# Kernel tuning notes

Measured on AMD Instinct MI355X. Metric: run time of the kernel, lower is better.

The kernel has to match this reference:

```python
import jax, jax.numpy as jnp
import numpy as np

N_ORDERS = 2
CHUNK = 64            # real tokens per chunk
LINEAR_ACTIVATION = False
STAB = 10000.0


def _ensure_stability(x):
    x = jnp.clip(x, -STAB, STAB)
    return jnp.nan_to_num(x, nan=0.0, posinf=STAB, neginf=-STAB)


def setup_inputs() -> dict:
    key = jax.random.key(0)
    k1, k2, k3, k4 = jax.random.split(key, 4)
    B, H, NC, D = 2, 16, 32, 128
    CT = CHUNK * N_ORDERS  # 128 virtual tokens per chunk
    s = 1.0 / np.sqrt(D)
    q_chunks = jax.random.normal(k1, (B, H, NC, CT, D), jnp.float32) * s
    W = jax.random.normal(k2, (B, H, NC, CT, D), jnp.float32) * s
    U = jax.random.normal(k3, (B, H, NC, CT, D), jnp.float32) * s
    h0 = jax.random.normal(k4, (B, H, D, D), jnp.float32) * s
    return {"q_chunks": q_chunks, "W": W, "U": U, "h0": h0}


def _gelu_norm(h):
    # h_norm/2 * gelu(2*h/h_norm, tanh) applied to chunk-boundary state
    n = jnp.linalg.norm(h, axis=-1, keepdims=True) + 1e-6
    return n / 2.0 * jax.nn.gelu(2.0 * h / n, approximate=True)


def _delta_product_scan(q_chunks, W, U, h0):
    B, H, NC, CT, D = q_chunks.shape
    C = CT // N_ORDERS

    def body(h, chunk):
        q_c, w_c, u_c = chunk  # each [B,H,CT,D]
        # virtual-token layout: token c, step s lives at index c*n_orders+s
        qs = q_c.reshape(B, H, C, N_ORDERS, D)
        ws = w_c.reshape(B, H, C, N_ORDERS, D)
        us = u_c.reshape(B, H, C, N_ORDERS, D)
        state = jnp.broadcast_to(h[:, :, None], (B, H, C, D, D))  # per-token state
        outs = []
        for step in range(N_ORDERS):
            q_s = qs[:, :, :, step]
            w_s = ws[:, :, :, step]
            u_s = us[:, :, :, step]
            k_trans_h = jnp.einsum('bhcd,bhcde->bhce', w_s, state)
            u_val = u_s - k_trans_h
            o_inter = jnp.einsum('bhcd,bhcde->bhce', q_s, state)
            o_intra = q_s * u_val  # elementwise, as in source
            outs.append(o_intra + o_inter)
            state = _ensure_stability(state + w_s[..., :, None] * u_val[..., None, :])
        out = jnp.stack(outs, axis=3).reshape(B, H, CT, D)
        h_new = state[:, :, -1]
        if not LINEAR_ACTIVATION:
            h_new = _gelu_norm(h_new)
        return h_new, out

    chunks = (jnp.moveaxis(q_chunks, 2, 0), jnp.moveaxis(W, 2, 0), jnp.moveaxis(U, 2, 0))
    h_final, ys = jax.lax.scan(body, h0, chunks)
    return jnp.moveaxis(ys, 0, 2), h_final  # [B,H,NC,CT,D], [B,H,D,D]


def reference(q_chunks, W, U, h0):
    return _delta_product_scan(q_chunks, W, U, h0)
```

## Files before the change

kernel.cpp:

```cpp
#include <hip/hip_runtime.h>


#define Dd 128
#define NCH 32
#define YS 16777216

typedef __attribute__((ext_vector_type(4))) float floatx4;
typedef __attribute__((ext_vector_type(8))) short short8;

__device__ __forceinline__ unsigned cvtpk(float lo, float hi) {
  unsigned r;
  asm("v_cvt_pk_bf16_f32 %0, %1, %2" : "=v"(r) : "v"(lo), "v"(hi));
  return r;
}

__global__ __launch_bounds__(512) void p1_scan(const float* __restrict__ W,
    const float* __restrict__ U, const float* __restrict__ h0,
    unsigned short* __restrict__ hws, float* __restrict__ out) {
  __shared__ float wpre[NCH * 320];
  __shared__ float upre[NCH * 2 * Dd];
  __shared__ float d10pre[NCH];
  __shared__ float sqb[Dd * 129];
  __shared__ float nrm2[4 * 40];

  const int bh = blockIdx.x;
  const int t = threadIdx.x;
  const int w = t >> 6, l = t & 63;
  const int c = (w << 4) | (l & 15);
  const int rg = l >> 4;

  {
    const float* Wg = W + (size_t)bh * NCH * 16384;
    const float* Ug = U + (size_t)bh * NCH * 16384;
#pragma unroll
    for (int k = 0; k < 4; k++) {
      int idx4 = k * 512 + t;
      int n = idx4 >> 6;
      int rem = idx4 & 63;
      int r = rem >> 5, e4 = (rem & 31) * 4;
      size_t g = (size_t)n * 16384 + (size_t)(126 + r) * Dd + e4;
      *(float4*)&upre[idx4 * 4] = *(const float4*)&Ug[g];
      *(float4*)&wpre[n * 320 + r * 160 + (e4 >> 5) * 40 + (e4 & 31)] =
          *(const float4*)&Wg[g];
    }
  }
  {
    const float4* hg = (const float4*)(h0 + (size_t)bh * 16384);
#pragma unroll
    for (int k = 0; k < 8; k++) {
      int idx4 = k * 512 + t;
      float4 v = hg[idx4];
      int d = idx4 >> 5, e4 = (idx4 & 31) * 4;
      sqb[d * 129 + e4 + 0] = v.x;
      sqb[d * 129 + e4 + 1] = v.y;
      sqb[d * 129 + e4 + 2] = v.z;
      sqb[d * 129 + e4 + 3] = v.w;
    }
  }
  __syncthreads();
  {
    int n = t >> 4, j = t & 15;
    const float* w0p = &wpre[n * 320 + (j >> 2) * 40 + (j & 3) * 8];
    const float* w1p = w0p + 160;
    float p = 0.f;
#pragma unroll
    for (int i = 0; i < 8; i++) p += w0p[i] * w1p[i];
    p += __shfl_xor(p, 1, 64);
    p += __shfl_xor(p, 2, 64);
    p += __shfl_xor(p, 4, 64);
    p += __shfl_xor(p, 8, 64);
    if (j == 0) d10pre[n] = p;
  }
  float hr[32];
#pragma unroll
  for (int i = 0; i < 32; i++) hr[i] = sqb[(rg * 32 + i) * 129 + c];
  __syncthreads();

  const int cpos = (c & 96) | ((c + 8 * rg) & 31);
  float* sqw = &sqb[rg * 32 * 129 + cpos];
  const int srow = t >> 2, sst = t & 3;
  const float* sqr = &sqb[srow * 129 + sst * 32];

  unsigned short* hwsb = hws + (size_t)bh * NCH * 16384;
  {
    unsigned pk[16];
#pragma unroll
    for (int i = 0; i < 16; i++) pk[i] = cvtpk(hr[2 * i], hr[2 * i + 1]);
    uint4* dst = (uint4*)(hwsb + (size_t)c * Dd + rg * 32);
    dst[0] = make_uint4(pk[0], pk[1], pk[2], pk[3]);
    dst[1] = make_uint4(pk[4], pk[5], pk[6], pk[7]);
    dst[2] = make_uint4(pk[8], pk[9], pk[10], pk[11]);
    dst[3] = make_uint4(pk[12], pk[13], pk[14], pk[15]);
  }

  for (int n = 0; n < NCH; n++) {
    floatx4 w0v[8], w1v[8];
    const float* wb = &wpre[n * 320 + rg * 40];
#pragma unroll
    for (int i = 0; i < 8; i++) {
      w0v[i] = *(const floatx4*)&wb[4 * i];
      w1v[i] = *(const floatx4*)&wb[160 + 4 * i];
    }
    float a0 = 0.f, a1 = 0.f, b0 = 0.f, b1 = 0.f;
#pragma unroll
    for (int i = 0; i < 8; i += 2) {
#pragma unroll
      for (int j = 0; j < 4; j++) {
        float h0v = hr[4 * i + j];
        float h1v = hr[4 * i + 4 + j];
        a0 = fmaf(w0v[i][j], h0v, a0);
        a1 = fmaf(w1v[i][j], h0v, a1);
        b0 = fmaf(w0v[i + 1][j], h1v, b0);
        b1 = fmaf(w1v[i + 1][j], h1v, b1);
      }
    }
    a0 += b0; a1 += b1;
    a0 += __shfl_xor(a0, 16, 64);
    a0 += __shfl_xor(a0, 32, 64);
    a1 += __shfl_xor(a1, 16, 64);
    a1 += __shfl_xor(a1, 32, 64);
    const float u0 = upre[n * 256 + c];
    const float u1 = upre[n * 256 + Dd + c];
    const float d10 = d10pre[n];
    const float uv0 = u0 - a0;
    const float uv1 = u1 - a1 - d10 * uv0;
#pragma unroll
    for (int i = 0; i < 8; i++)
#pragma unroll
      for (int j = 0; j < 4; j++) {
        int ii = 4 * i + j;
        float s = __builtin_amdgcn_fmed3f(fmaf(w0v[i][j], uv0, hr[ii]),
                                          -10000.0f, 10000.0f);
        s = __builtin_amdgcn_fmed3f(fmaf(w1v[i][j], uv1, s),
                                    -10000.0f, 10000.0f);
        hr[ii] = s;
        sqw[ii * 129] = s;
      }
    __syncthreads();
    {
      float acc = 0.f, acc2 = 0.f;
#pragma unroll
      for (int b = 0; b < 4; b++) {
        const float* p = sqr + 8 * ((b + sst) & 3);
#pragma unroll
        for (int i = 0; i < 8; i += 2) {
          float v = p[i], v2 = p[i + 1];
          acc = fmaf(v, v, acc);
          acc2 = fmaf(v2, v2, acc2);
        }
      }
      acc += acc2;
      acc += __shfl_xor(acc, 1, 64);
      acc += __shfl_xor(acc, 2, 64);
      if (sst == 0) {
        float nd = sqrtf(acc) + 1e-6f;
        nrm2[(srow >> 5) * 40 + (srow & 31)] = __fdividef(2.0f, nd);
      }
    }
    __syncthreads();
    floatx4 r2v[8];
    const float* nb = &nrm2[rg * 40];
#pragma unroll
    for (int i = 0; i < 8; i++) r2v[i] = *(const floatx4*)&nb[4 * i];
#pragma unroll
    for (int i = 0; i < 8; i++)
#pragma unroll
      for (int j = 0; j < 4; j++) {
        int ii = 4 * i + j;
        float h = hr[ii];
        float x = h * r2v[i][j];
        float x2 = x * x;
        float aa = x * fmaf(0.071354816f, x2, 1.59576912f);
        float ex = __expf(-aa);
        hr[ii] = __fdividef(h, 1.0f + ex);
      }
    if (n < NCH - 1) {
      unsigned pk[16];
#pragma unroll
      for (int i = 0; i < 16; i++) pk[i] = cvtpk(hr[2 * i], hr[2 * i + 1]);
      uint4* dst = (uint4*)(hwsb + (size_t)(n + 1) * 16384 + (size_t)c * Dd + rg * 32);
      dst[0] = make_uint4(pk[0], pk[1], pk[2], pk[3]);
      dst[1] = make_uint4(pk[4], pk[5], pk[6], pk[7]);
      dst[2] = make_uint4(pk[8], pk[9], pk[10], pk[11]);
      dst[3] = make_uint4(pk[12], pk[13], pk[14], pk[15]);
    } else {
      float* ob = out + YS + (size_t)bh * 16384;
#pragma unroll
      for (int i = 0; i < 32; i++) ob[(rg * 32 + i) * Dd + c] = hr[i];
    }
  }
}


__device__ __forceinline__ void stage_slice(const float* Qb, const float* Wb,
    float* qd, float* wd, int kc, int wv6, int ln) {
#pragma unroll
  for (int i = 0; i < 4; i++) {
    int cb = i * 512 + wv6 * 64;
    int isW = cb >> 10;
    int cbm = cb & 1023;
    int c = cbm + ln;
    int r = c >> 3;
    int s = (c >> 4) & 7;
    const float* g = (isW ? Wb : Qb) + r * Dd + kc * 32 + (((c & 7) ^ s) << 2);
    float* l = (isW ? wd : qd) + (cbm << 2);
    __builtin_amdgcn_global_load_lds(
        (const __attribute__((address_space(1))) void*)g,
        (__attribute__((address_space(3))) void*)l, 16, 0, 0);
  }
}

__global__ __launch_bounds__(512, 1) void p2_out(const float* __restrict__ Q,
    const float* __restrict__ W, const float* __restrict__ U,
    const unsigned short* __restrict__ hws, float* __restrict__ out) {
  __shared__ unsigned short hT[Dd * 136];
  __shared__ float qsl[2][4096];
  __shared__ float wsl[2][4096];
  __shared__ float d10s[64], dq1s[64];
  __shared__ float dps[512];

  const int bid = blockIdx.x;
  const int n = bid & 31, bh = bid >> 5;
  const size_t base = (size_t)(bh * NCH + n) * 16384;
  const float* Qb = Q + base;
  const float* Wb = W + base;
  const float* Ub = U + base;
  float* Ob = out + base;
  const int t = threadIdx.x;
  const int wv6 = t >> 6, ln = t & 63;

  stage_slice(Qb, Wb, &qsl[0][0], &wsl[0][0], 0, wv6, ln);

  {
    const uint4* src = (const uint4*)(hws + base);
#pragma unroll
    for (int i = 0; i < 4; i++) {
      int idx = t + i * 512;
      uint4 v = src[idx];
      int e = idx >> 4, j = idx & 15;
      *(uint4*)&hT[e * 136 + j * 8] = v;
    }
  }
  {
    int which = t >> 8, tt = t & 255;
    int cc = tt >> 2, part = tt & 3;
    const float4* ar = (const float4*)((which ? Qb : Wb) + (2 * cc + 1) * Dd + part * 32);
    const float4* w0r = (const float4*)(Wb + (2 * cc) * Dd + part * 32);
    float s = 0.f;
#pragma unroll
    for (int i = 0; i < 8; i++) {
      float4 a = ar[i], b = w0r[i];
      s += a.x * b.x + a.y * b.y + a.z * b.z + a.w * b.w;
    }
    dps[which * 256 + tt] = s;
  }
  __syncthreads();
  if (t < 128) {
    int which = t >> 6, cc = t & 63;
    const float* p = dps + which * 256 + cc * 4;
    float s = p[0] + p[1] + p[2] + p[3];
    (which ? dq1s : d10s)[cc] = s;
  }

  const int pr = wv6 >> 2, eq = wv6 & 3;
  const int lm = ln & 15, lq = ln >> 4;
  const int sw = lm & 7;
  const int i0 = ((2 * lq) ^ sw) << 2;
  const int i1 = ((2 * lq + 1) ^ sw) << 2;

  floatx4 acc[3][4][2];
#pragma unroll
  for (int m = 0; m < 3; m++)
#pragma unroll
    for (int ci = 0; ci < 4; ci++)
#pragma unroll
      for (int j = 0; j < 2; j++) acc[m][ci][j] = (floatx4){0.f, 0.f, 0.f, 0.f};

  int cur = 0;
  for (int kc = 0; kc < 4; kc++) {
    if (kc < 3)
      stage_slice(Qb, Wb, &qsl[cur ^ 1][0], &wsl[cur ^ 1][0], kc + 1, wv6, ln);
    const int k0 = kc * 32;
    short8 bfr[2];
#pragma unroll
    for (int j = 0; j < 2; j++) {
      int ee = (2 * eq + j) * 16 + lm;
      bfr[j] = *(const short8*)&hT[ee * 136 + k0 + 8 * lq];
    }
    const float* qs = &qsl[cur][0];
    const float* ws = &wsl[cur][0];
#pragma unroll
    for (int ci = 0; ci < 4; ci++) {
      const int rb = (32 * ci + 2 * lm) * 32;
      {
        const float* p = qs + rb + pr * 32;
        floatx4 g0 = *(const floatx4*)(p + i0);
        floatx4 g1 = *(const floatx4*)(p + i1);
        union { short8 v; unsigned u[4]; } af;
        af.u[0] = cvtpk(g0[0], g0[1]);
        af.u[1] = cvtpk(g0[2], g0[3]);
        af.u[2] = cvtpk(g1[0], g1[1]);
        af.u[3] = cvtpk(g1[2], g1[3]);
        acc[0][ci][0] = __builtin_amdgcn_mfma_f32_16x16x32_bf16(af.v, bfr[0], acc[0][ci][0], 0, 0, 0);
        acc[0][ci][1] = __builtin_amdgcn_mfma_f32_16x16x32_bf16(af.v, bfr[1], acc[0][ci][1], 0, 0, 0);
      }
      {
        const float* p = ws + rb + pr * 32;
        floatx4 g0 = *(const floatx4*)(p + i0);
        floatx4 g1 = *(const floatx4*)(p + i1);
        union { short8 v; unsigned u[4]; } af;
        af.u[0] = cvtpk(g0[0], g0[1]);
        af.u[1] = cvtpk(g0[2], g0[3]);
        af.u[2] = cvtpk(g1[0], g1[1]);
        af.u[3] = cvtpk(g1[2], g1[3]);
        acc[1][ci][0] = __builtin_amdgcn_mfma_f32_16x16x32_bf16(af.v, bfr[0], acc[1][ci][0], 0, 0, 0);
        acc[1][ci][1] = __builtin_amdgcn_mfma_f32_16x16x32_bf16(af.v, bfr[1], acc[1][ci][1], 0, 0, 0);
      }
      if (pr) {
        const float* p = ws + rb;
        floatx4 g0 = *(const floatx4*)(p + i0);
        floatx4 g1 = *(const floatx4*)(p + i1);
        union { short8 v; unsigned u[4]; } af;
        af.u[0] = cvtpk(g0[0], g0[1]);
        af.u[1] = cvtpk(g0[2], g0[3]);
        af.u[2] = cvtpk(g1[0], g1[1]);
        af.u[3] = cvtpk(g1[2], g1[3]);
        acc[2][ci][0] = __builtin_amdgcn_mfma_f32_16x16x32_bf16(af.v, bfr[0], acc[2][ci][0], 0, 0, 0);
        acc[2][ci][1] = __builtin_amdgcn_mfma_f32_16x16x32_bf16(af.v, bfr[1], acc[2][ci][1], 0, 0, 0);
      }
    }
    __syncthreads();
    cur ^= 1;
  }

  if (pr == 0) {
#pragma unroll
    for (int ci = 0; ci < 4; ci++)
#pragma unroll
      for (int j = 0; j < 2; j++) {
        int ee = (2 * eq + j) * 16 + lm;
#pragma unroll
        for (int r = 0; r < 4; r++) {
          int cc = ci * 16 + lq * 4 + r;
          float T0 = acc[1][ci][j][r];
          float Q0h = acc[0][ci][j][r];
          float u0 = Ub[(2 * cc) * Dd + ee];
          float q0 = Qb[(2 * cc) * Dd + ee];
          float uv0 = u0 - T0;
          Ob[(2 * cc) * Dd + ee] = q0 * uv0 + Q0h;
        }
      }
  } else {
#pragma unroll
    for (int ci = 0; ci < 4; ci++)
#pragma unroll
      for (int j = 0; j < 2; j++) {
        int ee = (2 * eq + j) * 16 + lm;
#pragma unroll
        for (int r = 0; r < 4; r++) {
          int cc = ci * 16 + lq * 4 + r;
          float T1 = acc[1][ci][j][r];
          float Q1h = acc[0][ci][j][r];
          float T0 = acc[2][ci][j][r];
          float u0 = Ub[(2 * cc) * Dd + ee];
          float u1 = Ub[(2 * cc + 1) * Dd + ee];
          float q1 = Qb[(2 * cc + 1) * Dd + ee];
          float uv0 = u0 - T0;
          float uv1 = u1 - T1 - d10s[cc] * uv0;
          Ob[(2 * cc + 1) * Dd + ee] = q1 * uv1 + Q1h + dq1s[cc] * uv0;
        }
      }
  }
}

extern "C" void kernel_launch(void* const* d_in, const int* in_sizes, int n_in,
                              void* d_out, int out_size, void* d_ws, size_t ws_size,
                              hipStream_t stream) {
  const float* Q = (const float*)d_in[0];
  const float* W = (const float*)d_in[1];
  const float* U = (const float*)d_in[2];
  const float* h0 = (const float*)d_in[3];
  float* out = (float*)d_out;
  unsigned short* hws = (unsigned short*)d_ws;

  p1_scan<<<32, 512, 0, stream>>>(W, U, h0, hws, out);
  p2_out<<<1024, 512, 0, stream>>>(Q, W, U, hws, out);
}
```

Measured before the change: 383.3 us.

## Fuse scan and output into persistent kernel with per-chunk readiness flags

Replaces the two launches with one persistent kernel. The first 32 blocks run the sequential state scan and publish a per-(bh, chunk) release flag once each chunk's bf16 state is written. The remaining blocks, and the scan blocks once they finish, pull output tiles in chunk-major order from an atomic work counter and spin on the flags, so output work overlaps the serial scan instead of waiting for it. Smaller changes ride along: W/U boundary rows are prefetched per chunk with global_load_lds, the w0·w1 dot product is computed inline, and the third MFMA accumulator is dropped by sharing uv0 through LDS. The costs are single-buffered Q/W staging, cross-block spin-waiting, and a memset of the flag area in the workspace; correctness depends on every block being resident at once.

```diff
diff --git a/kernel.cpp b/kernel.cpp
--- a/kernel.cpp
+++ b/kernel.cpp
@@ -4,6 +4,7 @@
 #define Dd 128
 #define NCH 32
 #define YS 16777216
+#define NTILES 1024
 
 typedef __attribute__((ext_vector_type(4))) float floatx4;
 typedef __attribute__((ext_vector_type(8))) short short8;
@@ -13,184 +14,25 @@
   asm("v_cvt_pk_bf16_f32 %0, %1, %2" : "=v"(r) : "v"(lo), "v"(hi));
   return r;
 }
-
-__global__ __launch_bounds__(512) void p1_scan(const float* __restrict__ W,
-    const float* __restrict__ U, const float* __restrict__ h0,
-    unsigned short* __restrict__ hws, float* __restrict__ out) {
-  __shared__ float wpre[NCH * 320];
-  __shared__ float upre[NCH * 2 * Dd];
-  __shared__ float d10pre[NCH];
-  __shared__ float sqb[Dd * 129];
-  __shared__ float nrm2[4 * 40];
-
-  const int bh = blockIdx.x;
-  const int t = threadIdx.x;
-  const int w = t >> 6, l = t & 63;
-  const int c = (w << 4) | (l & 15);
-  const int rg = l >> 4;
-
-  {
-    const float* Wg = W + (size_t)bh * NCH * 16384;
-    const float* Ug = U + (size_t)bh * NCH * 16384;
-#pragma unroll
-    for (int k = 0; k < 4; k++) {
-      int idx4 = k * 512 + t;
-      int n = idx4 >> 6;
-      int rem = idx4 & 63;
-      int r = rem >> 5, e4 = (rem & 31) * 4;
-      size_t g = (size_t)n * 16384 + (size_t)(126 + r) * Dd + e4;
-      *(float4*)&upre[idx4 * 4] = *(const float4*)&Ug[g];
-      *(float4*)&wpre[n * 320 + r * 160 + (e4 >> 5) * 40 + (e4 & 31)] =
-          *(const float4*)&Wg[g];
-    }
-  }
-  {
-    const float4* hg = (const float4*)(h0 + (size_t)bh * 16384);
-#pragma unroll
-    for (int k = 0; k < 8; k++) {
-      int idx4 = k * 512 + t;
-      float4 v = hg[idx4];
-      int d = idx4 >> 5, e4 = (idx4 & 31) * 4;
-      sqb[d * 129 + e4 + 0] = v.x;
-      sqb[d * 129 + e4 + 1] = v.y;
-      sqb[d * 129 + e4 + 2] = v.z;
-      sqb[d * 129 + e4 + 3] = v.w;
-    }
-  }
-  __syncthreads();
-  {
-    int n = t >> 4, j = t & 15;
-    const float* w0p = &wpre[n * 320 + (j >> 2) * 40 + (j & 3) * 8];
-    const float* w1p = w0p + 160;
-    float p = 0.f;
-#pragma unroll
-    for (int i = 0; i < 8; i++) p += w0p[i] * w1p[i];
-    p += __shfl_xor(p, 1, 64);
-    p += __shfl_xor(p, 2, 64);
-    p += __shfl_xor(p, 4, 64);
-    p += __shfl_xor(p, 8, 64);
-    if (j == 0) d10pre[n] = p;
-  }
-  float hr[32];
-#pragma unroll
-  for (int i = 0; i < 32; i++) hr[i] = sqb[(rg * 32 + i) * 129 + c];
-  __syncthreads();
-
-  const int cpos = (c & 96) | ((c + 8 * rg) & 31);
-  float* sqw = &sqb[rg * 32 * 129 + cpos];
-  const int srow = t >> 2, sst = t & 3;
-  const float* sqr = &sqb[srow * 129 + sst * 32];
-
-  unsigned short* hwsb = hws + (size_t)bh * NCH * 16384;
-  {
-    unsigned pk[16];
-#pragma unroll
-    for (int i = 0; i < 16; i++) pk[i] = cvtpk(hr[2 * i], hr[2 * i + 1]);
-    uint4* dst = (uint4*)(hwsb + (size_t)c * Dd + rg * 32);
-    dst[0] = make_uint4(pk[0], pk[1], pk[2], pk[3]);
-    dst[1] = make_uint4(pk[4], pk[5], pk[6], pk[7]);
-    dst[2] = make_uint4(pk[8], pk[9], pk[10], pk[11]);
-    dst[3] = make_uint4(pk[12], pk[13], pk[14], pk[15]);
-  }
-
-  for (int n = 0; n < NCH; n++) {
-    floatx4 w0v[8], w1v[8];
-    const float* wb = &wpre[n * 320 + rg * 40];
-#pragma unroll
-    for (int i = 0; i < 8; i++) {
-      w0v[i] = *(const floatx4*)&wb[4 * i];
-      w1v[i] = *(const floatx4*)&wb[160 + 4 * i];
-    }
-    float a0 = 0.f, a1 = 0.f, b0 = 0.f, b1 = 0.f;
-#pragma unroll
-    for (int i = 0; i < 8; i += 2) {
-#pragma unroll
-      for (int j = 0; j < 4; j++) {
-        float h0v = hr[4 * i + j];
-        float h1v = hr[4 * i + 4 + j];
-        a0 = fmaf(w0v[i][j], h0v, a0);
-        a1 = fmaf(w1v[i][j], h0v, a1);
-        b0 = fmaf(w0v[i + 1][j], h1v, b0);
-        b1 = fmaf(w1v[i + 1][j], h1v, b1);
-      }
-    }
-    a0 += b0; a1 += b1;
-    a0 += __shfl_xor(a0, 16, 64);
-    a0 += __shfl_xor(a0, 32, 64);
-    a1 += __shfl_xor(a1, 16, 64);
-    a1 += __shfl_xor(a1, 32, 64);
-    const float u0 = upre[n * 256 + c];
-    const float u1 = upre[n * 256 + Dd + c];
-    const float d10 = d10pre[n];
-    const float uv0 = u0 - a0;
-    const float uv1 = u1 - a1 - d10 * uv0;
-#pragma unroll
-    for (int i = 0; i < 8; i++)
-#pragma unroll
-      for (int j = 0; j < 4; j++) {
-        int ii = 4 * i + j;
-        float s = __builtin_amdgcn_fmed3f(fmaf(w0v[i][j], uv0, hr[ii]),
-                                          -10000.0f, 10000.0f);
-        s = __builtin_amdgcn_fmed3f(fmaf(w1v[i][j], uv1, s),
-                                    -10000.0f, 10000.0f);
-        hr[ii] = s;
-        sqw[ii * 129] = s;
-      }
-    __syncthreads();
-    {
-      float acc = 0.f, acc2 = 0.f;
-#pragma unroll
-      for (int b = 0; b < 4; b++) {
-        const float* p = sqr + 8 * ((b + sst) & 3);
-#pragma unroll
-        for (int i = 0; i < 8; i += 2) {
-          float v = p[i], v2 = p[i + 1];
-          acc = fmaf(v, v, acc);
-          acc2 = fmaf(v2, v2, acc2);
-        }
-      }
-      acc += acc2;
-      acc += __shfl_xor(acc, 1, 64);
-      acc += __shfl_xor(acc, 2, 64);
-      if (sst == 0) {
-        float nd = sqrtf(acc) + 1e-6f;
-        nrm2[(srow >> 5) * 40 + (srow & 31)] = __fdividef(2.0f, nd);
-      }
-    }
-    __syncthreads();
-    floatx4 r2v[8];
-    const float* nb = &nrm2[rg * 40];
-#pragma unroll
-    for (int i = 0; i < 8; i++) r2v[i] = *(const floatx4*)&nb[4 * i];
-#pragma unroll
-    for (int i = 0; i < 8; i++)
-#pragma unroll
-      for (int j = 0; j < 4; j++) {
-        int ii = 4 * i + j;
-        float h = hr[ii];
-        float x = h * r2v[i][j];
-        float x2 = x * x;
-        float aa = x * fmaf(0.071354816f, x2, 1.59576912f);
-        float ex = __expf(-aa);
-        hr[ii] = __fdividef(h, 1.0f + ex);
-      }
-    if (n < NCH - 1) {
-      unsigned pk[16];
-#pragma unroll
-      for (int i = 0; i < 16; i++) pk[i] = cvtpk(hr[2 * i], hr[2 * i + 1]);
-      uint4* dst = (uint4*)(hwsb + (size_t)(n + 1) * 16384 + (size_t)c * Dd + rg * 32);
-      dst[0] = make_uint4(pk[0], pk[1], pk[2], pk[3]);
-      dst[1] = make_uint4(pk[4], pk[5], pk[6], pk[7]);
-      dst[2] = make_uint4(pk[8], pk[9], pk[10], pk[11]);
-      dst[3] = make_uint4(pk[12], pk[13], pk[14], pk[15]);
-    } else {
-      float* ob = out + YS + (size_t)bh * 16384;
-#pragma unroll
-      for (int i = 0; i < 32; i++) ob[(rg * 32 + i) * Dd + c] = hr[i];
-    }
-  }
+__device__ __forceinline__ unsigned short f2bf(float f) {
+  unsigned int u = __float_as_uint(f);
+  u += 0x7fffu + ((u >> 16) & 1u);
+  return (unsigned short)(u >> 16);
 }
 
+struct SMemScan {
+  float wu[2][512];
+  float sqb[Dd * 129];
+  float nrm2[4 * 40];
+};
+struct SMemTile {
+  unsigned short hT[Dd * 136];
+  float qsl[4096];
+  float wsl[4096];
+  float d10s[64], dq1s[64];
+  float dps[512];
+};
+union SMemU { SMemScan s; SMemTile t; };
 
 __device__ __forceinline__ void stage_slice(const float* Qb, const float* Wb,
     float* qd, float* wd, int kc, int wv6, int ln) {
@@ -210,166 +52,343 @@
   }
 }
 
-__global__ __launch_bounds__(512, 1) void p2_out(const float* __restrict__ Q,
+__global__ __launch_bounds__(512, 4) void fused(const float* __restrict__ Q,
     const float* __restrict__ W, const float* __restrict__ U,
-    const unsigned short* __restrict__ hws, float* __restrict__ out) {
-  __shared__ unsigned short hT[Dd * 136];
-  __shared__ float qsl[2][4096];
-  __shared__ float wsl[2][4096];
-  __shared__ float d10s[64], dq1s[64];
-  __shared__ float dps[512];
-
+    const float* __restrict__ h0, unsigned short* __restrict__ hws,
+    float* __restrict__ out) {
+  __shared__ SMemU sm;
+  __shared__ int tsel;
+  int* flags = (int*)hws;
   const int bid = blockIdx.x;
-  const int n = bid & 31, bh = bid >> 5;
-  const size_t base = (size_t)(bh * NCH + n) * 16384;
-  const float* Qb = Q + base;
-  const float* Wb = W + base;
-  const float* Ub = U + base;
-  float* Ob = out + base;
   const int t = threadIdx.x;
+
+  if (bid < 32) {
+    const int bh = bid;
+    const int w = t >> 6, l = t & 63;
+    const int c = (w << 4) | (l & 15);
+    const int rg = l >> 4;
+    const float* Wbh = W + (size_t)bh * NCH * 16384;
+    const float* Ubh = U + (size_t)bh * NCH * 16384;
+
+    if (w == 0) {
+      int ord = l >> 5, q = l & 31;
+      const float* gw = Wbh + 126 * Dd + ord * Dd + (q & 3) * 32 + (q >> 2) * 4;
+      __builtin_amdgcn_global_load_lds(
+          (const __attribute__((address_space(1))) void*)gw,
+          (__attribute__((address_space(3))) void*)&sm.s.wu[0][0], 16, 0, 0);
+      const float* gu = Ubh + 126 * Dd + l * 4;
+      __builtin_amdgcn_global_load_lds(
+          (const __attribute__((address_space(1))) void*)gu,
+          (__attribute__((address_space(3))) void*)&sm.s.wu[0][256], 16, 0, 0);
+    }
+    {
+      const float4* hg = (const float4*)(h0 + (size_t)bh * 16384);
+#pragma unroll
+      for (int k = 0; k < 8; k++) {
+        int idx4 = k * 512 + t;
+        float4 v = hg[idx4];
+        int d = idx4 >> 5, e4 = (idx4 & 31) * 4;
+        sm.s.sqb[d * 129 + e4 + 0] = v.x;
+        sm.s.sqb[d * 129 + e4 + 1] = v.y;
+        sm.s.sqb[d * 129 + e4 + 2] = v.z;
+        sm.s.sqb[d * 129 + e4 + 3] = v.w;
+      }
+    }
+    __syncthreads();
+    float hr[32];
+#pragma unroll
+    for (int i = 0; i < 32; i++) hr[i] = sm.s.sqb[(rg * 32 + i) * 129 + c];
+    __syncthreads();
+
+    const int cpos = (c & 96) | ((c + 8 * rg) & 31);
+    float* sqw = &sm.s.sqb[rg * 32 * 129 + cpos];
+    const int srow = t >> 2, sst = t & 3;
+    const float* sqr = &sm.s.sqb[srow * 129 + sst * 32];
+    unsigned short* hwsb = hws + (size_t)bh * NCH * 16384;
+
+    for (int n = 0; n < NCH; n++) {
+      if (w == 0 && n + 1 < NCH) {
+        int ord = l >> 5, q = l & 31;
+        const float* gw = Wbh + (size_t)(n + 1) * 16384 + 126 * Dd + ord * Dd +
+                          (q & 3) * 32 + (q >> 2) * 4;
+        __builtin_amdgcn_global_load_lds(
+            (const __attribute__((address_space(1))) void*)gw,
+            (__attribute__((address_space(3))) void*)&sm.s.wu[(n + 1) & 1][0],
+            16, 0, 0);
+        const float* gu = Ubh + (size_t)(n + 1) * 16384 + 126 * Dd + l * 4;
+        __builtin_amdgcn_global_load_lds(
+            (const __attribute__((address_space(1))) void*)gu,
+            (__attribute__((address_space(3))) void*)&sm.s.wu[(n + 1) & 1][256],
+            16, 0, 0);
+      }
+      const float* wb = &sm.s.wu[n & 1][0];
+      floatx4 w0v[8], w1v[8];
+#pragma unroll
+      for (int i = 0; i < 8; i++) {
+        w0v[i] = *(const floatx4*)&wb[16 * i + 4 * rg];
+        w1v[i] = *(const floatx4*)&wb[128 + 16 * i + 4 * rg];
+      }
+      float a0 = 0.f, a1 = 0.f, b0 = 0.f, b1 = 0.f, dp = 0.f, dp2 = 0.f;
+#pragma unroll
+      for (int i = 0; i < 8; i += 2) {
+#pragma unroll
+        for (int j = 0; j < 4; j++) {
+          float h0v = hr[4 * i + j];
+          float h1v = hr[4 * i + 4 + j];
+          a0 = fmaf(w0v[i][j], h0v, a0);
+          a1 = fmaf(w1v[i][j], h0v, a1);
+          b0 = fmaf(w0v[i + 1][j], h1v, b0);
+          b1 = fmaf(w1v[i + 1][j], h1v, b1);
+          dp = fmaf(w0v[i][j], w1v[i][j], dp);
+          dp2 = fmaf(w0v[i + 1][j], w1v[i + 1][j], dp2);
+        }
+      }
+      a0 += b0; a1 += b1; dp += dp2;
+      a0 += __shfl_xor(a0, 16, 64);
+      a0 += __shfl_xor(a0, 32, 64);
+      a1 += __shfl_xor(a1, 16, 64);
+      a1 += __shfl_xor(a1, 32, 64);
+      dp += __shfl_xor(dp, 16, 64);
+      dp += __shfl_xor(dp, 32, 64);
+      const float u0 = wb[256 + c];
+      const float u1 = wb[384 + c];
+      const float uv0 = u0 - a0;
+      const float uv1 = u1 - a1 - dp * uv0;
+#pragma unroll
+      for (int i = 0; i < 8; i++)
+#pragma unroll
+        for (int j = 0; j < 4; j++) {
+          int ii = 4 * i + j;
+          float s = __builtin_amdgcn_fmed3f(fmaf(w0v[i][j], uv0, hr[ii]),
+                                            -10000.0f, 10000.0f);
+          s = __builtin_amdgcn_fmed3f(fmaf(w1v[i][j], uv1, s),
+                                      -10000.0f, 10000.0f);
+          hr[ii] = s;
+          sqw[ii * 129] = s;
+        }
+      __syncthreads();
+      if (t == 0 && n >= 1)
+        __hip_atomic_store(&flags[bh * 32 + n], 1, __ATOMIC_RELEASE,
+                           __HIP_MEMORY_SCOPE_AGENT);
+      {
+        float acc = 0.f, acc2 = 0.f;
+#pragma unroll
+        for (int b = 0; b < 4; b++) {
+          const float* p = sqr + 8 * ((b + sst) & 3);
+#pragma unroll
+          for (int i = 0; i < 8; i += 2) {
+            float v = p[i], v2 = p[i + 1];
+            acc = fmaf(v, v, acc);
+            acc2 = fmaf(v2, v2, acc2);
+          }
+        }
+        acc += acc2;
+        acc += __shfl_xor(acc, 1, 64);
+        acc += __shfl_xor(acc, 2, 64);
+        if (sst == 0) {
+          float nd = sqrtf(acc) + 1e-6f;
+          sm.s.nrm2[(srow >> 5) * 40 + (srow & 31)] = __fdividef(2.0f, nd);
+        }
+      }
+      __syncthreads();
+      floatx4 r2v[8];
+      const float* nb = &sm.s.nrm2[rg * 40];
+#pragma unroll
+      for (int i = 0; i < 8; i++) r2v[i] = *(const floatx4*)&nb[4 * i];
+#pragma unroll
+      for (int i = 0; i < 8; i++)
+#pragma unroll
+        for (int j = 0; j < 4; j++) {
+          int ii = 4 * i + j;
+          float h = hr[ii];
+          float x = h * r2v[i][j];
+          float x2 = x * x;
+          float aa = x * fmaf(0.071354816f, x2, 1.59576912f);
+          float ex = __expf(-aa);
+          hr[ii] = __fdividef(h, 1.0f + ex);
+        }
+      if (n < NCH - 1) {
+        unsigned pk[16];
+#pragma unroll
+        for (int i = 0; i < 16; i++) pk[i] = cvtpk(hr[2 * i], hr[2 * i + 1]);
+        uint4* dst = (uint4*)(hwsb + (size_t)(n + 1) * 16384 +
+                              (size_t)c * Dd + rg * 32);
+        dst[0] = make_uint4(pk[0], pk[1], pk[2], pk[3]);
+        dst[1] = make_uint4(pk[4], pk[5], pk[6], pk[7]);
+        dst[2] = make_uint4(pk[8], pk[9], pk[10], pk[11]);
+        dst[3] = make_uint4(pk[12], pk[13], pk[14], pk[15]);
+      } else {
+        float* ob = out + YS + (size_t)bh * 16384;
+#pragma unroll
+        for (int i = 0; i < 32; i++) ob[(rg * 32 + i) * Dd + c] = hr[i];
+      }
+    }
+  }
+
   const int wv6 = t >> 6, ln = t & 63;
-
-  stage_slice(Qb, Wb, &qsl[0][0], &wsl[0][0], 0, wv6, ln);
-
-  {
-    const uint4* src = (const uint4*)(hws + base);
-#pragma unroll
-    for (int i = 0; i < 4; i++) {
-      int idx = t + i * 512;
-      uint4 v = src[idx];
-      int e = idx >> 4, j = idx & 15;
-      *(uint4*)&hT[e * 136 + j * 8] = v;
-    }
-  }
-  {
-    int which = t >> 8, tt = t & 255;
-    int cc = tt >> 2, part = tt & 3;
-    const float4* ar = (const float4*)((which ? Qb : Wb) + (2 * cc + 1) * Dd + part * 32);
-    const float4* w0r = (const float4*)(Wb + (2 * cc) * Dd + part * 32);
-    float s = 0.f;
-#pragma unroll
-    for (int i = 0; i < 8; i++) {
-      float4 a = ar[i], b = w0r[i];
-      s += a.x * b.x + a.y * b.y + a.z * b.z + a.w * b.w;
-    }
-    dps[which * 256 + tt] = s;
-  }
-  __syncthreads();
-  if (t < 128) {
-    int which = t >> 6, cc = t & 63;
-    const float* p = dps + which * 256 + cc * 4;
-    float s = p[0] + p[1] + p[2] + p[3];
-    (which ? dq1s : d10s)[cc] = s;
-  }
-
   const int pr = wv6 >> 2, eq = wv6 & 3;
   const int lm = ln & 15, lq = ln >> 4;
   const int sw = lm & 7;
   const int i0 = ((2 * lq) ^ sw) << 2;
   const int i1 = ((2 * lq + 1) ^ sw) << 2;
 
-  floatx4 acc[3][4][2];
-#pragma unroll
-  for (int m = 0; m < 3; m++)
-#pragma unroll
-    for (int ci = 0; ci < 4; ci++)
-#pragma unroll
-      for (int j = 0; j < 2; j++) acc[m][ci][j] = (floatx4){0.f, 0.f, 0.f, 0.f};
-
-  int cur = 0;
-  for (int kc = 0; kc < 4; kc++) {
-    if (kc < 3)
-      stage_slice(Qb, Wb, &qsl[cur ^ 1][0], &wsl[cur ^ 1][0], kc + 1, wv6, ln);
-    const int k0 = kc * 32;
-    short8 bfr[2];
-#pragma unroll
-    for (int j = 0; j < 2; j++) {
-      int ee = (2 * eq + j) * 16 + lm;
-      bfr[j] = *(const short8*)&hT[ee * 136 + k0 + 8 * lq];
-    }
-    const float* qs = &qsl[cur][0];
-    const float* ws = &wsl[cur][0];
-#pragma unroll
-    for (int ci = 0; ci < 4; ci++) {
-      const int rb = (32 * ci + 2 * lm) * 32;
-      {
-        const float* p = qs + rb + pr * 32;
-        floatx4 g0 = *(const floatx4*)(p + i0);
-        floatx4 g1 = *(const floatx4*)(p + i1);
-        union { short8 v; unsigned u[4]; } af;
-        af.u[0] = cvtpk(g0[0], g0[1]);
-        af.u[1] = cvtpk(g0[2], g0[3]);
-        af.u[2] = cvtpk(g1[0], g1[1]);
-        af.u[3] = cvtpk(g1[2], g1[3]);
-        acc[0][ci][0] = __builtin_amdgcn_mfma_f32_16x16x32_bf16(af.v, bfr[0], acc[0][ci][0], 0, 0, 0);
-        acc[0][ci][1] = __builtin_amdgcn_mfma_f32_16x16x32_bf16(af.v, bfr[1], acc[0][ci][1], 0, 0, 0);
-      }
-      {
-        const float* p = ws + rb + pr * 32;
-        floatx4 g0 = *(const floatx4*)(p + i0);
-        floatx4 g1 = *(const floatx4*)(p + i1);
-        union { short8 v; unsigned u[4]; } af;
-        af.u[0] = cvtpk(g0[0], g0[1]);
-        af.u[1] = cvtpk(g0[2], g0[3]);
-        af.u[2] = cvtpk(g1[0], g1[1]);
-        af.u[3] = cvtpk(g1[2], g1[3]);
-        acc[1][ci][0] = __builtin_amdgcn_mfma_f32_16x16x32_bf16(af.v, bfr[0], acc[1][ci][0], 0, 0, 0);
-        acc[1][ci][1] = __builtin_amdgcn_mfma_f32_16x16x32_bf16(af.v, bfr[1], acc[1][ci][1], 0, 0, 0);
-      }
-      if (pr) {
-        const float* p = ws + rb;
-        floatx4 g0 = *(const floatx4*)(p + i0);
-        floatx4 g1 = *(const floatx4*)(p + i1);
-        union { short8 v; unsigned u[4]; } af;
-        af.u[0] = cvtpk(g0[0], g0[1]);
-        af.u[1] = cvtpk(g0[2], g0[3]);
-        af.u[2] = cvtpk(g1[0], g1[1]);
-        af.u[3] = cvtpk(g1[2], g1[3]);
-        acc[2][ci][0] = __builtin_amdgcn_mfma_f32_16x16x32_bf16(af.v, bfr[0], acc[2][ci][0], 0, 0, 0);
-        acc[2][ci][1] = __builtin_amdgcn_mfma_f32_16x16x32_bf16(af.v, bfr[1], acc[2][ci][1], 0, 0, 0);
-      }
-    }
-    __syncthreads();
-    cur ^= 1;
-  }
-
-  if (pr == 0) {
-#pragma unroll
-    for (int ci = 0; ci < 4; ci++)
+  while (true) {
+    __syncthreads();
+    if (t == 0) tsel = atomicAdd(&flags[1024], 1);
+    __syncthreads();
+    const int tt = tsel;
+    if (tt >= NTILES) break;
+    const int n = tt >> 5, bh = tt & 31;
+    const size_t base = (size_t)(bh * NCH + n) * 16384;
+    const float* Qb = Q + base;
+    const float* Wb = W + base;
+    const float* Ub = U + base;
+    float* Ob = out + base;
+
+    stage_slice(Qb, Wb, &sm.t.qsl[0], &sm.t.wsl[0], 0, wv6, ln);
+    {
+      int which = t >> 8, t2 = t & 255;
+      int cc = t2 >> 2, part = t2 & 3;
+      const float4* ar =
+          (const float4*)((which ? Qb : Wb) + (2 * cc + 1) * Dd + part * 32);
+      const float4* w0r = (const float4*)(Wb + (2 * cc) * Dd + part * 32);
+      float s = 0.f;
+#pragma unroll
+      for (int i = 0; i < 8; i++) {
+        float4 a = ar[i], b = w0r[i];
+        s += a.x * b.x + a.y * b.y + a.z * b.z + a.w * b.w;
+      }
+      sm.t.dps[which * 256 + t2] = s;
+    }
+    if (n > 0 && t == 0) {
+      while (__hip_atomic_load(&flags[bh * 32 + n], __ATOMIC_RELAXED,
+                               __HIP_MEMORY_SCOPE_AGENT) == 0)
+        __builtin_amdgcn_s_sleep(32);
+      (void)__hip_atomic_load(&flags[bh * 32 + n], __ATOMIC_ACQUIRE,
+                              __HIP_MEMORY_SCOPE_AGENT);
+    }
+    __syncthreads();
+    if (t < 128) {
+      int which = t >> 6, cc = t & 63;
+      const float* p = sm.t.dps + which * 256 + cc * 4;
+      float s = p[0] + p[1] + p[2] + p[3];
+      (which ? sm.t.dq1s : sm.t.d10s)[cc] = s;
+    }
+    if (n == 0) {
+      const float* h0b = h0 + (size_t)bh * 16384;
+#pragma unroll
+      for (int i = 0; i < 8; i++) {
+        int idx4 = t + i * 512;
+        float4 v = ((const float4*)h0b)[idx4];
+        int d = idx4 >> 5, e4 = (idx4 & 31) * 4;
+        sm.t.hT[(e4 + 0) * 136 + d] = f2bf(v.x);
+        sm.t.hT[(e4 + 1) * 136 + d] = f2bf(v.y);
+        sm.t.hT[(e4 + 2) * 136 + d] = f2bf(v.z);
+        sm.t.hT[(e4 + 3) * 136 + d] = f2bf(v.w);
+      }
+    } else {
+      const uint4* src = (const uint4*)(hws + base);
+#pragma unroll
+      for (int i = 0; i < 4; i++) {
+        int idx = t + i * 512;
+        uint4 v = src[idx];
+        int e = idx >> 4, j = idx & 15;
+        *(uint4*)&sm.t.hT[e * 136 + j * 8] = v;
+      }
+    }
+    __syncthreads();
+
+    floatx4 acc[2][4][2];
+#pragma unroll
+    for (int m = 0; m < 2; m++)
+#pragma unroll
+      for (int ci = 0; ci < 4; ci++)
+#pragma unroll
+        for (int j = 0; j < 2; j++) acc[m][ci][j] = (floatx4){0.f, 0.f, 0.f, 0.f};
+
+    for (int kc = 0; kc < 4; kc++) {
+      const int k0 = kc * 32;
+      short8 bfr[2];
 #pragma unroll
       for (int j = 0; j < 2; j++) {
         int ee = (2 * eq + j) * 16 + lm;
-#pragma unroll
-        for (int r = 0; r < 4; r++) {
-          int cc = ci * 16 + lq * 4 + r;
-          float T0 = acc[1][ci][j][r];
-          float Q0h = acc[0][ci][j][r];
-          float u0 = Ub[(2 * cc) * Dd + ee];
-          float q0 = Qb[(2 * cc) * Dd + ee];
-          float uv0 = u0 - T0;
-          Ob[(2 * cc) * Dd + ee] = q0 * uv0 + Q0h;
-        }
-      }
-  } else {
-#pragma unroll
-    for (int ci = 0; ci < 4; ci++)
-#pragma unroll
-      for (int j = 0; j < 2; j++) {
-        int ee = (2 * eq + j) * 16 + lm;
-#pragma unroll
-        for (int r = 0; r < 4; r++) {
-          int cc = ci * 16 + lq * 4 + r;
-          float T1 = acc[1][ci][j][r];
-          float Q1h = acc[0][ci][j][r];
-          float T0 = acc[2][ci][j][r];
-          float u0 = Ub[(2 * cc) * Dd + ee];
-          float u1 = Ub[(2 * cc + 1) * Dd + ee];
-          float q1 = Qb[(2 * cc + 1) * Dd + ee];
-          float uv0 = u0 - T0;
-          float uv1 = u1 - T1 - d10s[cc] * uv0;
-          Ob[(2 * cc + 1) * Dd + ee] = q1 * uv1 + Q1h + dq1s[cc] * uv0;
-        }
-      }
+        bfr[j] = *(const short8*)&sm.t.hT[ee * 136 + k0 + 8 * lq];
+      }
+#pragma unroll
+      for (int ci = 0; ci < 4; ci++) {
+        const int rb = (32 * ci + 2 * lm) * 32 + pr * 32;
+        {
+          const float* p = &sm.t.qsl[rb];
+          floatx4 g0 = *(const floatx4*)(p + i0);
+          floatx4 g1 = *(const floatx4*)(p + i1);
+          union { short8 v; unsigned u[4]; } af;
+          af.u[0] = cvtpk(g0[0], g0[1]);
+          af.u[1] = cvtpk(g0[2], g0[3]);
+          af.u[2] = cvtpk(g1[0], g1[1]);
+          af.u[3] = cvtpk(g1[2], g1[3]);
+          acc[0][ci][0] = __builtin_amdgcn_mfma_f32_16x16x32_bf16(af.v, bfr[0], acc[0][ci][0], 0, 0, 0);
+          acc[0][ci][1] = __builtin_amdgcn_mfma_f32_16x16x32_bf16(af.v, bfr[1], acc[0][ci][1], 0, 0, 0);
+        }
+        {
+          const float* p = &sm.t.wsl[rb];
+          floatx4 g0 = *(const floatx4*)(p + i0);
+          floatx4 g1 = *(const floatx4*)(p + i1);
+          union { short8 v; unsigned u[4]; } af;
+          af.u[0] = cvtpk(g0[0], g0[1]);
+          af.u[1] = cvtpk(g0[2], g0[3]);
+          af.u[2] = cvtpk(g1[0], g1[1]);
+          af.u[3] = cvtpk(g1[2], g1[3]);
+          acc[1][ci][0] = __builtin_amdgcn_mfma_f32_16x16x32_bf16(af.v, bfr[0], acc[1][ci][0], 0, 0, 0);
+          acc[1][ci][1] = __builtin_amdgcn_mfma_f32_16x16x32_bf16(af.v, bfr[1], acc[1][ci][1], 0, 0, 0);
+        }
+      }
+      __syncthreads();
+      if (kc < 3) {
+        stage_slice(Qb, Wb, &sm.t.qsl[0], &sm.t.wsl[0], kc + 1, wv6, ln);
+        __syncthreads();
+      }
+    }
+
+    float* uv0s = (float*)sm.t.hT;
+    if (pr == 0) {
+#pragma unroll
+      for (int ci = 0; ci < 4; ci++)
+#pragma unroll
+        for (int j = 0; j < 2; j++) {
+          int ee = (2 * eq + j) * 16 + lm;
+#pragma unroll
+          for (int r = 0; r < 4; r++) {
+            int cc = ci * 16 + lq * 4 + r;
+            float T0 = acc[1][ci][j][r];
+            float Q0h = acc[0][ci][j][r];
+            float u0 = Ub[(2 * cc) * Dd + ee];
+            float q0 = Qb[(2 * cc) * Dd + ee];
+            float uv0 = u0 - T0;
+            uv0s[cc * Dd + ee] = uv0;
+            Ob[(2 * cc) * Dd + ee] = q0 * uv0 + Q0h;
+          }
+        }
+    }
+    __syncthreads();
+    if (pr == 1) {
+#pragma unroll
+      for (int ci = 0; ci < 4; ci++)
+#pragma unroll
+        for (int j = 0; j < 2; j++) {
+          int ee = (2 * eq + j) * 16 + lm;
+#pragma unroll
+          for (int r = 0; r < 4; r++) {
+            int cc = ci * 16 + lq * 4 + r;
+            float T1 = acc[1][ci][j][r];
+            float Q1h = acc[0][ci][j][r];
+            float u1 = Ub[(2 * cc + 1) * Dd + ee];
+            float q1 = Qb[(2 * cc + 1) * Dd + ee];
+            float uv0 = uv0s[cc * Dd + ee];
+            float uv1 = u1 - T1 - sm.t.d10s[cc] * uv0;
+            Ob[(2 * cc + 1) * Dd + ee] = q1 * uv1 + Q1h + sm.t.dq1s[cc] * uv0;
+          }
+        }
+    }
   }
 }
 
@@ -383,6 +402,6 @@
   float* out = (float*)d_out;
   unsigned short* hws = (unsigned short*)d_ws;
 
-  p1_scan<<<32, 512, 0, stream>>>(W, U, h0, hws, out);
-  p2_out<<<1024, 512, 0, stream>>>(Q, W, U, hws, out);
+  hipMemsetAsync(d_ws, 0, 8192, stream);
+  fused<<<512, 512, 0, stream>>>(Q, W, U, h0, hws, out);
 }
```

Measured after the change: 477.2 us. 1.24x slower.
